# Kernel optimization log

Hardware: AMD Instinct MI355X
Metric: run time of the kernel (lower is better)

The kernel has to match this reference:

```python
import jax, jax.numpy as jnp
import numpy as np


def setup_inputs() -> dict:
    key = jax.random.key(0)
    k1, k2, k3 = jax.random.split(key, 3)
    shape = (16, 128, 128, 64)  # [B, H, W, C]
    return {
        "query": jax.random.normal(k1, shape, dtype=jnp.float32),
        "keys": jax.random.normal(k2, shape, dtype=jnp.float32),
        "values": jax.random.normal(k3, shape, dtype=jnp.float32),
    }


def reference(query, keys, values):
    # Attention over channel dim C, feature dim = H*W.
    # scores[b, q, k] = sum_{h,w} Q[b,h,w,q] * K[b,h,w,k]
    scores = jnp.einsum("bhwq,bhwk->bqk", query, keys)
    attn = jax.nn.softmax(scores, axis=-1)  # softmax over keys k
    # out[b,h,w,q] = sum_k attn[b,q,k] * V[b,h,w,k]
    out = jnp.einsum("bqk,bhwk->bhwq", attn, values)
    return out
```

## Files before the change

kernel.cpp:

```cpp
#include <hip/hip_runtime.h>


#define TILE_ROWS 32

template <int SPLIT>
__global__ __launch_bounds__(256) void scores_kernel(
    const float* __restrict__ Q, const float* __restrict__ K,
    float* __restrict__ partial) {
  constexpr int CH = 16384 / SPLIT;
  constexpr int NT = CH / TILE_ROWS;
  const int bs = blockIdx.x;
  const int b = bs / SPLIT;
  const int s = bs % SPLIT;
  const int tid = threadIdx.x;
  const int w = tid >> 6;
  const int l = tid & 63;
  const int q0 = (l >> 3) * 8;
  const int k0 = (l & 7) * 8;

  __shared__ union {
    struct { float4 q[2][512]; float4 k[2][512]; } t;
    float red[2][4096];
  } lds;

  float acc[8][8];
#pragma unroll
  for (int i = 0; i < 8; ++i)
#pragma unroll
    for (int j = 0; j < 8; ++j) acc[i][j] = 0.f;

  const float4* Qg = (const float4*)(Q + ((size_t)b * 16384 + (size_t)s * CH) * 64);
  const float4* Kg = (const float4*)(K + ((size_t)b * 16384 + (size_t)s * CH) * 64);

  lds.t.q[0][tid]       = Qg[tid];
  lds.t.q[0][tid + 256] = Qg[tid + 256];
  lds.t.k[0][tid]       = Kg[tid];
  lds.t.k[0][tid + 256] = Kg[tid + 256];

  for (int t = 0; t < NT; ++t) {
    __syncthreads();
    const int cb = t & 1;

    float4 pq0, pq1, pk0, pk1;
    if (t + 1 < NT) {
      pq0 = Qg[(t + 1) * 512 + tid];
      pq1 = Qg[(t + 1) * 512 + tid + 256];
      pk0 = Kg[(t + 1) * 512 + tid];
      pk1 = Kg[(t + 1) * 512 + tid + 256];
    }

#pragma unroll
    for (int i = 0; i < 8; ++i) {
      const int r = (i << 2) + w;
      float4 qa = lds.t.q[cb][r * 16 + (q0 >> 2)];
      float4 qb = lds.t.q[cb][r * 16 + (q0 >> 2) + 1];
      float4 ka = lds.t.k[cb][r * 16 + (k0 >> 2)];
      float4 kb = lds.t.k[cb][r * 16 + (k0 >> 2) + 1];
      float qv[8] = {qa.x, qa.y, qa.z, qa.w, qb.x, qb.y, qb.z, qb.w};
      float kv[8] = {ka.x, ka.y, ka.z, ka.w, kb.x, kb.y, kb.z, kb.w};
#pragma unroll
      for (int ii = 0; ii < 8; ++ii)
#pragma unroll
        for (int jj = 0; jj < 8; ++jj)
          acc[ii][jj] += qv[ii] * kv[jj];
    }

    if (t + 1 < NT) {
      const int nb = (t + 1) & 1;
      lds.t.q[nb][tid]       = pq0;
      lds.t.q[nb][tid + 256] = pq1;
      lds.t.k[nb][tid]       = pk0;
      lds.t.k[nb][tid + 256] = pk1;
    }
  }

  __syncthreads();
  if (w >= 2) {
    float4* dst = (float4*)lds.red[w - 2];
#pragma unroll
    for (int i = 0; i < 8; ++i) {
      dst[(q0 + i) * 16 + (k0 >> 2)]     = make_float4(acc[i][0], acc[i][1], acc[i][2], acc[i][3]);
      dst[(q0 + i) * 16 + (k0 >> 2) + 1] = make_float4(acc[i][4], acc[i][5], acc[i][6], acc[i][7]);
    }
  }
  __syncthreads();
  if (w < 2) {
    float4* dst = (float4*)lds.red[w];
#pragma unroll
    for (int i = 0; i < 8; ++i) {
      float4 u = dst[(q0 + i) * 16 + (k0 >> 2)];
      float4 v = dst[(q0 + i) * 16 + (k0 >> 2) + 1];
      dst[(q0 + i) * 16 + (k0 >> 2)]     = make_float4(u.x + acc[i][0], u.y + acc[i][1], u.z + acc[i][2], u.w + acc[i][3]);
      dst[(q0 + i) * 16 + (k0 >> 2) + 1] = make_float4(v.x + acc[i][4], v.y + acc[i][5], v.z + acc[i][6], v.w + acc[i][7]);
    }
  }
  __syncthreads();
  float4* p4 = (float4*)(partial + (size_t)bs * 4096);
  const float4* r0 = (const float4*)lds.red[0];
  const float4* r1 = (const float4*)lds.red[1];
#pragma unroll
  for (int c = 0; c < 4; ++c) {
    float4 x = r0[c * 256 + tid];
    float4 y = r1[c * 256 + tid];
    p4[c * 256 + tid] = make_float4(x.x + y.x, x.y + y.y, x.z + y.z, x.w + y.w);
  }
}

template <int SPLIT>
__global__ __launch_bounds__(256) void softmax_kernel(
    const float* __restrict__ partial, float* __restrict__ attn_t) {
  const int blk = blockIdx.x;
  const int b = blk >> 4;
  const int q0 = (blk & 15) * 4;
  const int tid = threadIdx.x;
  const int w = tid >> 6;
  const int l = tid & 63;
  const int ql = l >> 4;
  const int k4 = l & 15;

  __shared__ float4 red4[4][64];

  const float4* P = (const float4*)partial;
  float4 v = make_float4(0.f, 0.f, 0.f, 0.f);
  for (int s = w; s < SPLIT; s += 4) {
    float4 t = P[((size_t)(b * SPLIT + s) * 64 + q0 + ql) * 16 + k4];
    v.x += t.x; v.y += t.y; v.z += t.z; v.w += t.w;
  }
  red4[w][l] = v;
  __syncthreads();
  if (w != 0) return;

  float4 v1 = red4[1][l], v2 = red4[2][l], v3 = red4[3][l];
  v.x += v1.x + v2.x + v3.x;
  v.y += v1.y + v2.y + v3.y;
  v.z += v1.z + v2.z + v3.z;
  v.w += v1.w + v2.w + v3.w;

  float m = fmaxf(fmaxf(v.x, v.y), fmaxf(v.z, v.w));
#pragma unroll
  for (int off = 8; off > 0; off >>= 1)
    m = fmaxf(m, __shfl_xor(m, off, 64));
  float4 e = make_float4(__expf(v.x - m), __expf(v.y - m), __expf(v.z - m), __expf(v.w - m));
  float sum = e.x + e.y + e.z + e.w;
#pragma unroll
  for (int off = 8; off > 0; off >>= 1)
    sum += __shfl_xor(sum, off, 64);
  const float inv = 1.f / sum;

  float* A = attn_t + (size_t)b * 4096;
  A[(4 * k4 + 0) * 64 + q0 + ql] = e.x * inv;
  A[(4 * k4 + 1) * 64 + q0 + ql] = e.y * inv;
  A[(4 * k4 + 2) * 64 + q0 + ql] = e.z * inv;
  A[(4 * k4 + 3) * 64 + q0 + ql] = e.w * inv;
}

__global__ __launch_bounds__(256) void out_kernel(
    const float* __restrict__ V, const float* __restrict__ attn_t,
    float* __restrict__ out) {
  const int b = blockIdx.x >> 7;
  const int tile = blockIdx.x & 127;
  const int tid = threadIdx.x;
  const int g = tid >> 4;
  const int qg = tid & 15;

  __shared__ float4 Vl[128 * 17];
  __shared__ float4 Al[64 * 16];

  const float4* Vg = (const float4*)(V + ((size_t)b * 16384 + (size_t)tile * 128) * 64);
#pragma unroll
  for (int u = 0; u < 8; ++u) {
    const int idx = u * 256 + tid;
    Vl[(idx >> 4) * 17 + (idx & 15)] = Vg[idx];
  }
  const float4* Ag = (const float4*)(attn_t + (size_t)b * 4096);
#pragma unroll
  for (int u = 0; u < 4; ++u)
    Al[u * 256 + tid] = Ag[u * 256 + tid];
  __syncthreads();

  float acc[8][4];
#pragma unroll
  for (int i = 0; i < 8; ++i)
#pragma unroll
    for (int j = 0; j < 4; ++j) acc[i][j] = 0.f;

  for (int k4 = 0; k4 < 16; ++k4) {
    const float4 a0 = Al[(4 * k4 + 0) * 16 + qg];
    const float4 a1 = Al[(4 * k4 + 1) * 16 + qg];
    const float4 a2 = Al[(4 * k4 + 2) * 16 + qg];
    const float4 a3 = Al[(4 * k4 + 3) * 16 + qg];
#pragma unroll
    for (int i = 0; i < 8; ++i) {
      const float4 v = Vl[(i * 16 + g) * 17 + k4];
      acc[i][0] += v.x * a0.x + v.y * a1.x + v.z * a2.x + v.w * a3.x;
      acc[i][1] += v.x * a0.y + v.y * a1.y + v.z * a2.y + v.w * a3.y;
      acc[i][2] += v.x * a0.z + v.y * a1.z + v.z * a2.z + v.w * a3.z;
      acc[i][3] += v.x * a0.w + v.y * a1.w + v.z * a2.w + v.w * a3.w;
    }
  }

  float4* og = (float4*)(out + ((size_t)b * 16384 + (size_t)tile * 128) * 64);
#pragma unroll
  for (int i = 0; i < 8; ++i) {
    const int row = i * 16 + g;
    og[row * 16 + qg] = make_float4(acc[i][0], acc[i][1], acc[i][2], acc[i][3]);
  }
}

extern "C" void kernel_launch(void* const* d_in, const int* in_sizes, int n_in,
                              void* d_out, int out_size, void* d_ws, size_t ws_size,
                              hipStream_t stream) {
  const float* Q = (const float*)d_in[0];
  const float* K = (const float*)d_in[1];
  const float* V = (const float*)d_in[2];
  float* out = (float*)d_out;

  const size_t need64 = (size_t)16 * 64 * 4096 * 4 + (size_t)16 * 4096 * 4;

  if (ws_size >= need64) {
    float* partial = (float*)d_ws;
    float* attn_t = partial + (size_t)16 * 64 * 4096;
    scores_kernel<64><<<16 * 64, 256, 0, stream>>>(Q, K, partial);
    softmax_kernel<64><<<16 * 16, 256, 0, stream>>>(partial, attn_t);
    out_kernel<<<16 * 128, 256, 0, stream>>>(V, attn_t, out);
  } else {
    float* partial = (float*)d_ws;
    float* attn_t = partial + (size_t)16 * 32 * 4096;
    scores_kernel<32><<<16 * 32, 256, 0, stream>>>(Q, K, partial);
    softmax_kernel<32><<<16 * 16, 256, 0, stream>>>(partial, attn_t);
    out_kernel<<<16 * 128, 256, 0, stream>>>(V, attn_t, out);
  }
}
```

Measured before the change: 234.5 us.

## Use wave-private LDS buffers in scores and enlarge out-kernel register tile

In the scores kernel each wave now loads and double-buffers only the rows it consumes into its own LDS slice. That removes the block-wide __syncthreads from the main loop. In the output kernel each block now covers 256 spatial rows and each thread an 8x8 output tile, reading V through an XOR-swizzled LDS layout. This raises FMA work per LDS read and avoids bank conflicts, but the larger LDS footprint (about 80KB) lowers occupancy and the launch now uses half as many blocks.

```diff
diff --git a/kernel.cpp b/kernel.cpp
--- a/kernel.cpp
+++ b/kernel.cpp
@@ -19,7 +19,7 @@
   const int k0 = (l & 7) * 8;
 
   __shared__ union {
-    struct { float4 q[2][512]; float4 k[2][512]; } t;
+    float4 buf[4][2][256];
     float red[2][4096];
   } lds;
 
@@ -32,30 +32,35 @@
   const float4* Qg = (const float4*)(Q + ((size_t)b * 16384 + (size_t)s * CH) * 64);
   const float4* Kg = (const float4*)(K + ((size_t)b * 16384 + (size_t)s * CH) * 64);
 
-  lds.t.q[0][tid]       = Qg[tid];
-  lds.t.q[0][tid + 256] = Qg[tid + 256];
-  lds.t.k[0][tid]       = Kg[tid];
-  lds.t.k[0][tid + 256] = Kg[tid + 256];
+  const int i0 = l >> 4;
+  const int c0 = l & 15;
+  const int gq0 = (4 * i0 + w) * 16 + c0;
+  const int gq1 = gq0 + 256;
+
+  lds.buf[w][0][l]       = Qg[gq0];
+  lds.buf[w][0][64 + l]  = Qg[gq1];
+  lds.buf[w][0][128 + l] = Kg[gq0];
+  lds.buf[w][0][192 + l] = Kg[gq1];
 
   for (int t = 0; t < NT; ++t) {
-    __syncthreads();
     const int cb = t & 1;
 
     float4 pq0, pq1, pk0, pk1;
     if (t + 1 < NT) {
-      pq0 = Qg[(t + 1) * 512 + tid];
-      pq1 = Qg[(t + 1) * 512 + tid + 256];
-      pk0 = Kg[(t + 1) * 512 + tid];
-      pk1 = Kg[(t + 1) * 512 + tid + 256];
-    }
-
-#pragma unroll
-    for (int i = 0; i < 8; ++i) {
-      const int r = (i << 2) + w;
-      float4 qa = lds.t.q[cb][r * 16 + (q0 >> 2)];
-      float4 qb = lds.t.q[cb][r * 16 + (q0 >> 2) + 1];
-      float4 ka = lds.t.k[cb][r * 16 + (k0 >> 2)];
-      float4 kb = lds.t.k[cb][r * 16 + (k0 >> 2) + 1];
+      pq0 = Qg[(t + 1) * 512 + gq0];
+      pq1 = Qg[(t + 1) * 512 + gq1];
+      pk0 = Kg[(t + 1) * 512 + gq0];
+      pk1 = Kg[(t + 1) * 512 + gq1];
+    }
+
+    const float4* qp = lds.buf[w][cb];
+    const float4* kp = lds.buf[w][cb] + 128;
+#pragma unroll
+    for (int i = 0; i < 8; ++i) {
+      float4 qa = qp[i * 16 + (q0 >> 2)];
+      float4 qb = qp[i * 16 + (q0 >> 2) + 1];
+      float4 ka = kp[i * 16 + (k0 >> 2)];
+      float4 kb = kp[i * 16 + (k0 >> 2) + 1];
       float qv[8] = {qa.x, qa.y, qa.z, qa.w, qb.x, qb.y, qb.z, qb.w};
       float kv[8] = {ka.x, ka.y, ka.z, ka.w, kb.x, kb.y, kb.z, kb.w};
 #pragma unroll
@@ -67,10 +72,10 @@
 
     if (t + 1 < NT) {
       const int nb = (t + 1) & 1;
-      lds.t.q[nb][tid]       = pq0;
-      lds.t.q[nb][tid + 256] = pq1;
-      lds.t.k[nb][tid]       = pk0;
-      lds.t.k[nb][tid + 256] = pk1;
+      lds.buf[w][nb][l]       = pq0;
+      lds.buf[w][nb][64 + l]  = pq1;
+      lds.buf[w][nb][128 + l] = pk0;
+      lds.buf[w][nb][192 + l] = pk1;
     }
   }
 
@@ -157,20 +162,23 @@
 __global__ __launch_bounds__(256) void out_kernel(
     const float* __restrict__ V, const float* __restrict__ attn_t,
     float* __restrict__ out) {
-  const int b = blockIdx.x >> 7;
-  const int tile = blockIdx.x & 127;
+  const int b = blockIdx.x >> 6;
+  const int tile = blockIdx.x & 63;
   const int tid = threadIdx.x;
-  const int g = tid >> 4;
-  const int qg = tid & 15;
-
-  __shared__ float4 Vl[128 * 17];
+  const int w = tid >> 6;
+  const int l = tid & 63;
+  const int rg = l >> 3;
+  const int qg = l & 7;
+
+  __shared__ float4 Vl[256 * 16];
   __shared__ float4 Al[64 * 16];
 
-  const float4* Vg = (const float4*)(V + ((size_t)b * 16384 + (size_t)tile * 128) * 64);
-#pragma unroll
-  for (int u = 0; u < 8; ++u) {
-    const int idx = u * 256 + tid;
-    Vl[(idx >> 4) * 17 + (idx & 15)] = Vg[idx];
+  const float4* Vg = (const float4*)(V + ((size_t)b * 16384 + (size_t)tile * 256) * 64);
+#pragma unroll
+  for (int u = 0; u < 16; ++u) {
+    const int n = u * 256 + tid;
+    const int r = n >> 4, c = n & 15;
+    Vl[(r << 4) | (c ^ (r & 7))] = Vg[n];
   }
   const float4* Ag = (const float4*)(attn_t + (size_t)b * 4096);
 #pragma unroll
@@ -178,32 +186,41 @@
     Al[u * 256 + tid] = Ag[u * 256 + tid];
   __syncthreads();
 
-  float acc[8][4];
+  float acc[8][8];
 #pragma unroll
   for (int i = 0; i < 8; ++i)
 #pragma unroll
-    for (int j = 0; j < 4; ++j) acc[i][j] = 0.f;
-
+    for (int j = 0; j < 8; ++j) acc[i][j] = 0.f;
+
+#pragma unroll 2
   for (int k4 = 0; k4 < 16; ++k4) {
-    const float4 a0 = Al[(4 * k4 + 0) * 16 + qg];
-    const float4 a1 = Al[(4 * k4 + 1) * 16 + qg];
-    const float4 a2 = Al[(4 * k4 + 2) * 16 + qg];
-    const float4 a3 = Al[(4 * k4 + 3) * 16 + qg];
-#pragma unroll
-    for (int i = 0; i < 8; ++i) {
-      const float4 v = Vl[(i * 16 + g) * 17 + k4];
-      acc[i][0] += v.x * a0.x + v.y * a1.x + v.z * a2.x + v.w * a3.x;
-      acc[i][1] += v.x * a0.y + v.y * a1.y + v.z * a2.y + v.w * a3.y;
-      acc[i][2] += v.x * a0.z + v.y * a1.z + v.z * a2.z + v.w * a3.z;
-      acc[i][3] += v.x * a0.w + v.y * a1.w + v.z * a2.w + v.w * a3.w;
-    }
-  }
-
-  float4* og = (float4*)(out + ((size_t)b * 16384 + (size_t)tile * 128) * 64);
+    float4 alo[4], ahi[4];
+#pragma unroll
+    for (int j = 0; j < 4; ++j) {
+      alo[j] = Al[(4 * k4 + j) * 16 + qg];
+      ahi[j] = Al[(4 * k4 + j) * 16 + 8 + qg];
+    }
+#pragma unroll
+    for (int i = 0; i < 8; ++i) {
+      const int row = (w << 6) + rg + 8 * i;
+      const float4 v = Vl[(row << 4) | (k4 ^ rg)];
+      acc[i][0] += v.x * alo[0].x + v.y * alo[1].x + v.z * alo[2].x + v.w * alo[3].x;
+      acc[i][1] += v.x * alo[0].y + v.y * alo[1].y + v.z * alo[2].y + v.w * alo[3].y;
+      acc[i][2] += v.x * alo[0].z + v.y * alo[1].z + v.z * alo[2].z + v.w * alo[3].z;
+      acc[i][3] += v.x * alo[0].w + v.y * alo[1].w + v.z * alo[2].w + v.w * alo[3].w;
+      acc[i][4] += v.x * ahi[0].x + v.y * ahi[1].x + v.z * ahi[2].x + v.w * ahi[3].x;
+      acc[i][5] += v.x * ahi[0].y + v.y * ahi[1].y + v.z * ahi[2].y + v.w * ahi[3].y;
+      acc[i][6] += v.x * ahi[0].z + v.y * ahi[1].z + v.z * ahi[2].z + v.w * ahi[3].z;
+      acc[i][7] += v.x * ahi[0].w + v.y * ahi[1].w + v.z * ahi[2].w + v.w * ahi[3].w;
+    }
+  }
+
+  float4* og = (float4*)(out + ((size_t)b * 16384 + (size_t)tile * 256) * 64);
 #pragma unroll
   for (int i = 0; i < 8; ++i) {
-    const int row = i * 16 + g;
-    og[row * 16 + qg] = make_float4(acc[i][0], acc[i][1], acc[i][2], acc[i][3]);
+    const int row = (w << 6) + rg + 8 * i;
+    og[row * 16 + qg]     = make_float4(acc[i][0], acc[i][1], acc[i][2], acc[i][3]);
+    og[row * 16 + 8 + qg] = make_float4(acc[i][4], acc[i][5], acc[i][6], acc[i][7]);
   }
 }
 
@@ -222,12 +239,12 @@
     float* attn_t = partial + (size_t)16 * 64 * 4096;
     scores_kernel<64><<<16 * 64, 256, 0, stream>>>(Q, K, partial);
     softmax_kernel<64><<<16 * 16, 256, 0, stream>>>(partial, attn_t);
-    out_kernel<<<16 * 128, 256, 0, stream>>>(V, attn_t, out);
+    out_kernel<<<16 * 64, 256, 0, stream>>>(V, attn_t, out);
   } else {
     float* partial = (float*)d_ws;
     float* attn_t = partial + (size_t)16 * 32 * 4096;
     scores_kernel<32><<<16 * 32, 256, 0, stream>>>(Q, K, partial);
     softmax_kernel<32><<<16 * 16, 256, 0, stream>>>(partial, attn_t);
-    out_kernel<<<16 * 128, 256, 0, stream>>>(V, attn_t, out);
-  }
-}
+    out_kernel<<<16 * 64, 256, 0, stream>>>(V, attn_t, out);
+  }
+}
```

After: 237.4 us. About the same (+1.3%).
